# Performance work log

Measured on AMD Instinct MI355X. Metric: run time of the kernel, lower is better.

The kernel has to match this reference:

```python
import jax, jax.numpy as jnp
import numpy as np

MAX_DEG = 6


def neighbor_lookup(atoms, edges, maskvalue, include_self):
    # atoms: (B, A, F), edges: (B, A, D) with -1 padding
    B, A, F = atoms.shape
    D = edges.shape[-1]
    mask = edges >= 0
    idx = jnp.where(mask, edges, 0).reshape(B, A * D)
    g = jnp.take_along_axis(atoms, idx[:, :, None], axis=1).reshape(B, A, D, F)
    g = jnp.where(mask[..., None], g, maskvalue)
    if include_self:
        g = jnp.concatenate([atoms[:, :, None, :], g], axis=2)  # (B,A,D+1,F)
    return g


def graph_conv(atoms, bonds, edges, W, b):
    # W: (MAX_DEG, F_in+BF, C), b: (MAX_DEG, C)
    deg = (edges >= 0).sum(-1)  # (B, A)
    summed_atoms = neighbor_lookup(atoms, edges, 0.0, True).sum(2)  # self + neighbors
    summed_bonds = bonds.sum(2)
    feats = jnp.concatenate([summed_atoms, summed_bonds], axis=-1)
    out = jnp.zeros(feats.shape[:2] + (W.shape[-1],), feats.dtype)
    for d in range(MAX_DEG):  # small fixed loop over degrees
        h = jax.nn.relu(feats @ W[d] + b[d])
        out = out + jnp.where((deg == d)[..., None], h, 0.0)
    return out


def graph_pool(atoms, edges):
    g = neighbor_lookup(atoms, edges, -jnp.inf, True)  # self included -> finite max
    return g.max(axis=2)


def graph_output(atoms, bonds, edges, Wo, bo):
    deg = (edges >= 0).sum(-1)
    feats = jnp.concatenate([atoms, bonds.sum(2)], axis=-1)
    out = jax.nn.softmax(feats @ Wo + bo, axis=-1)
    mask = (deg != 0)[..., None]  # zero out padded atoms
    return jnp.where(mask, out, 0.0).sum(axis=1)  # (B, hid)


def setup_inputs():
    key = jax.random.key(0)
    ks = jax.random.split(key, 16)
    B, A, D = 4096, 64, 6
    AF, BF, H = 37, 6, 128
    s = lambda k, sh: (jax.random.normal(k, sh, jnp.float32) * 0.05)
    return {
        "atoms": jax.random.normal(ks[0], (B, A, AF), jnp.float32),
        "bonds": jax.random.normal(ks[1], (B, A, D, BF), jnp.float32),
        "edges": jax.random.randint(ks[2], (B, A, D), -1, A),
        "W1": s(ks[3], (MAX_DEG, AF + BF, H)),
        "b1": s(ks[4], (MAX_DEG, H)),
        "W2": s(ks[5], (MAX_DEG, H + BF, H)),
        "b2": s(ks[6], (MAX_DEG, H)),
        "Wo": s(ks[7], (H + BF, H)),
        "bo": s(ks[8], (H,)),
        "Wm1": s(ks[9], (H, H // 2)),
        "bm1": s(ks[10], (H // 2,)),
        "Wm2": s(ks[11], (H // 2, H // 4)),
        "bm2": s(ks[12], (H // 4,)),
        "Wm3": s(ks[13], (H // 4, 1)),
        "bm3": s(ks[14], (1,)),
    }


def reference(atoms, bonds, edges, W1, b1, W2, b2, Wo, bo, Wm1, bm1, Wm2, bm2, Wm3, bm3):
    x = graph_conv(atoms, bonds, edges, W1, b1)
    x = graph_pool(x, edges)
    x = graph_conv(x, bonds, edges, W2, b2)
    x = graph_pool(x, edges)
    fp = graph_output(x, bonds, edges, Wo, bo)
    h = jax.nn.relu(fp @ Wm1 + bm1)
    h = jax.nn.relu(h @ Wm2 + bm2)
    out = (h @ Wm3 + bm3).squeeze()  # (B,)
    return out
```

## Files before the change

kernel.cpp:

```cpp
#include <hip/hip_runtime.h>
#include <math.h>


__device__ __forceinline__ float4 max4(float4 a, float4 b) {
  return make_float4(fmaxf(a.x, b.x), fmaxf(a.y, b.y), fmaxf(a.z, b.z), fmaxf(a.w, b.w));
}

__device__ __forceinline__ float4 nbr_max(const float4* sx4, const int* se, int a, int c4) {
  float4 m = sx4[a * 32 + c4];
#pragma unroll
  for (int d = 0; d < 6; ++d) {
    int e = se[a * 6 + d];
    if (e >= 0) m = max4(m, sx4[e * 32 + c4]);
  }
  return m;
}

__device__ __forceinline__ float4 nbr_sum(const float4* sx4, const int* se, int a, int c4) {
  float4 s = sx4[a * 32 + c4];
#pragma unroll
  for (int d = 0; d < 6; ++d) {
    int e = se[a * 6 + d];
    if (e >= 0) {
      float4 v = sx4[e * 32 + c4];
      s.x += v.x; s.y += v.y; s.z += v.z; s.w += v.w;
    }
  }
  return s;
}

__device__ __forceinline__ float4 nbr_wmax(const float4* sx4, const int* se, const int* sdeg,
                                           int a, int c4) {
  float4 m = make_float4(0.f, 0.f, 0.f, 0.f);
  if (sdeg[a] < 6) m = max4(m, sx4[a * 32 + c4]);
#pragma unroll
  for (int d = 0; d < 6; ++d) {
    int e = se[a * 6 + d];
    if (e >= 0 && sdeg[e] < 6) m = max4(m, sx4[e * 32 + c4]);
  }
  return m;
}

__global__ __launch_bounds__(256, 4) void qsar_fused(
    const float* __restrict__ atoms, const float* __restrict__ bonds,
    const int* __restrict__ edges,
    const float* __restrict__ W1, const float* __restrict__ b1,
    const float* __restrict__ W2, const float* __restrict__ b2,
    const float* __restrict__ Wo, const float* __restrict__ bo,
    const float* __restrict__ Wm1, const float* __restrict__ bm1,
    const float* __restrict__ Wm2, const float* __restrict__ bm2,
    const float* __restrict__ Wm3, const float* __restrict__ bm3,
    float* __restrict__ out)
{
  const int b    = blockIdx.x;
  const int tid  = threadIdx.x;
  const int lane = tid & 63;
  const int wid  = tid >> 6;

  __shared__ float s_x[64 * 128];
  __shared__ float s_sa[16 * 38];
  __shared__ float s_bsum[64 * 8];
  __shared__ int   s_edges[64 * 6];
  __shared__ int   s_deg[64];
  __shared__ int   s_work[64];
  __shared__ int   s_perm[64];
  __shared__ float s_rsum[64];
  __shared__ int   s_nwork, s_na, s_nz;

  float4* sx4  = reinterpret_cast<float4*>(s_x);
  float*  s_fp = s_sa;
  float*  s_h1 = s_sa + 256;
  float*  s_h2 = s_sa + 320;

  {
    const int* ge = edges + (size_t)b * (64 * 6);
    for (int i = tid; i < 64 * 6; i += 256) s_edges[i] = ge[i];
    const float* gb = bonds + (size_t)b * (64 * 36);
    for (int i = tid; i < 64 * 6; i += 256) {
      int a = i / 6, f = i - a * 6;
      float s = 0.f;
#pragma unroll
      for (int d = 0; d < 6; ++d) s += gb[a * 36 + d * 6 + f];
      s_bsum[a * 8 + f] = s;
    }
#pragma unroll
    for (int j = 0; j < 8; ++j) sx4[tid + j * 256] = make_float4(0.f, 0.f, 0.f, 0.f);
    if (tid == 0) { s_nwork = 0; s_na = 0; s_nz = 0; }
  }
  __syncthreads();

  if (tid < 64) {
    int dcnt = 0;
#pragma unroll
    for (int d = 0; d < 6; ++d) dcnt += (s_edges[tid * 6 + d] >= 0) ? 1 : 0;
    s_deg[tid] = dcnt;
    if (dcnt < 6) { int p = atomicAdd(&s_nwork, 1); s_work[p] = tid; }
  }
  __syncthreads();

  if (tid < 64) {
    int nzf = (s_deg[tid] < 6) ? 1 : 0;
#pragma unroll
    for (int d = 0; d < 6; ++d) {
      int e = s_edges[tid * 6 + d];
      if (e >= 0 && s_deg[e] < 6) nzf = 1;
    }
    if (nzf) { int p = atomicAdd(&s_na, 1); s_perm[p] = tid; }
    else     { int p = atomicAdd(&s_nz, 1); s_perm[63 - p] = tid; }
  }

  {
    const int nw = s_nwork;
    const float* ga = atoms + (size_t)b * (64 * 37);
    for (int cb = 0; cb < nw; cb += 16) {
      const int cnt = (nw - cb < 16) ? (nw - cb) : 16;
      for (int i = tid; i < cnt * 37; i += 256) {
        int wi = i / 37, k = i - wi * 37;
        int a = s_work[cb + wi];
        float f = ga[a * 37 + k];
#pragma unroll
        for (int d = 0; d < 6; ++d) {
          int e = s_edges[a * 6 + d];
          if (e >= 0) f += ga[e * 37 + k];
        }
        s_sa[wi * 38 + k] = f;
      }
      __syncthreads();
      for (int w = wid; w < cnt; w += 4) {
        const int a = s_work[cb + w];
        const int d = s_deg[a];
        const float* wp = W1 + d * (43 * 128);
        float2 bb = *reinterpret_cast<const float2*>(&b1[d * 128 + 2 * lane]);
        float acc0 = bb.x, acc1 = bb.y;
        for (int k = 0; k < 37; ++k) {
          float f = s_sa[w * 38 + k];
          float2 w2 = *reinterpret_cast<const float2*>(&wp[k * 128 + 2 * lane]);
          acc0 = fmaf(f, w2.x, acc0); acc1 = fmaf(f, w2.y, acc1);
        }
#pragma unroll
        for (int kk = 0; kk < 6; ++kk) {
          float f = s_bsum[a * 8 + kk];
          float2 w2 = *reinterpret_cast<const float2*>(&wp[(37 + kk) * 128 + 2 * lane]);
          acc0 = fmaf(f, w2.x, acc0); acc1 = fmaf(f, w2.y, acc1);
        }
        *reinterpret_cast<float2*>(&s_x[a * 128 + 2 * lane]) =
            make_float2(fmaxf(acc0, 0.f), fmaxf(acc1, 0.f));
      }
      __syncthreads();
    }
  }
  __syncthreads();

  {
    float4 v0 = nbr_max(sx4, s_edges, (tid + 0 * 256) >> 5, tid & 31);
    float4 v1 = nbr_max(sx4, s_edges, (tid + 1 * 256) >> 5, tid & 31);
    float4 v2 = nbr_max(sx4, s_edges, (tid + 2 * 256) >> 5, tid & 31);
    float4 v3 = nbr_max(sx4, s_edges, (tid + 3 * 256) >> 5, tid & 31);
    float4 v4 = nbr_max(sx4, s_edges, (tid + 4 * 256) >> 5, tid & 31);
    float4 v5 = nbr_max(sx4, s_edges, (tid + 5 * 256) >> 5, tid & 31);
    float4 v6 = nbr_max(sx4, s_edges, (tid + 6 * 256) >> 5, tid & 31);
    float4 v7 = nbr_max(sx4, s_edges, (tid + 7 * 256) >> 5, tid & 31);
    __syncthreads();
    sx4[tid + 0 * 256] = v0; sx4[tid + 1 * 256] = v1;
    sx4[tid + 2 * 256] = v2; sx4[tid + 3 * 256] = v3;
    sx4[tid + 4 * 256] = v4; sx4[tid + 5 * 256] = v5;
    sx4[tid + 6 * 256] = v6; sx4[tid + 7 * 256] = v7;
  }
  __syncthreads();

  {
    const float4 z = make_float4(0.f, 0.f, 0.f, 0.f);
    float4 v0 = z, v1 = z, v2 = z, v3 = z, v4 = z, v5 = z, v6 = z, v7 = z;
    if (s_deg[(tid + 0 * 256) >> 5] < 6) v0 = nbr_sum(sx4, s_edges, (tid + 0 * 256) >> 5, tid & 31);
    if (s_deg[(tid + 1 * 256) >> 5] < 6) v1 = nbr_sum(sx4, s_edges, (tid + 1 * 256) >> 5, tid & 31);
    if (s_deg[(tid + 2 * 256) >> 5] < 6) v2 = nbr_sum(sx4, s_edges, (tid + 2 * 256) >> 5, tid & 31);
    if (s_deg[(tid + 3 * 256) >> 5] < 6) v3 = nbr_sum(sx4, s_edges, (tid + 3 * 256) >> 5, tid & 31);
    if (s_deg[(tid + 4 * 256) >> 5] < 6) v4 = nbr_sum(sx4, s_edges, (tid + 4 * 256) >> 5, tid & 31);
    if (s_deg[(tid + 5 * 256) >> 5] < 6) v5 = nbr_sum(sx4, s_edges, (tid + 5 * 256) >> 5, tid & 31);
    if (s_deg[(tid + 6 * 256) >> 5] < 6) v6 = nbr_sum(sx4, s_edges, (tid + 6 * 256) >> 5, tid & 31);
    if (s_deg[(tid + 7 * 256) >> 5] < 6) v7 = nbr_sum(sx4, s_edges, (tid + 7 * 256) >> 5, tid & 31);
    __syncthreads();
    if (s_deg[(tid + 0 * 256) >> 5] < 6) sx4[tid + 0 * 256] = v0;
    if (s_deg[(tid + 1 * 256) >> 5] < 6) sx4[tid + 1 * 256] = v1;
    if (s_deg[(tid + 2 * 256) >> 5] < 6) sx4[tid + 2 * 256] = v2;
    if (s_deg[(tid + 3 * 256) >> 5] < 6) sx4[tid + 3 * 256] = v3;
    if (s_deg[(tid + 4 * 256) >> 5] < 6) sx4[tid + 4 * 256] = v4;
    if (s_deg[(tid + 5 * 256) >> 5] < 6) sx4[tid + 5 * 256] = v5;
    if (s_deg[(tid + 6 * 256) >> 5] < 6) sx4[tid + 6 * 256] = v6;
    if (s_deg[(tid + 7 * 256) >> 5] < 6) sx4[tid + 7 * 256] = v7;
  }
  __syncthreads();

  {
    const int nw = s_nwork;
    for (int w = wid; w < nw; w += 4) {
      const int a = s_work[w];
      const int d = s_deg[a];
      const float* wp = W2 + d * (134 * 128);
      float2 bb = *reinterpret_cast<const float2*>(&b2[d * 128 + 2 * lane]);
      float acc0 = bb.x, acc1 = bb.y;
      for (int k = 0; k < 128; ++k) {
        float f = s_x[a * 128 + k];
        float2 w2 = *reinterpret_cast<const float2*>(&wp[k * 128 + 2 * lane]);
        acc0 = fmaf(f, w2.x, acc0); acc1 = fmaf(f, w2.y, acc1);
      }
#pragma unroll
      for (int kk = 0; kk < 6; ++kk) {
        float f = s_bsum[a * 8 + kk];
        float2 w2 = *reinterpret_cast<const float2*>(&wp[(128 + kk) * 128 + 2 * lane]);
        acc0 = fmaf(f, w2.x, acc0); acc1 = fmaf(f, w2.y, acc1);
      }
      *reinterpret_cast<float2*>(&s_x[a * 128 + 2 * lane]) =
          make_float2(fmaxf(acc0, 0.f), fmaxf(acc1, 0.f));
    }
  }
  __syncthreads();

  {
    float4 v0 = nbr_wmax(sx4, s_edges, s_deg, (tid + 0 * 256) >> 5, tid & 31);
    float4 v1 = nbr_wmax(sx4, s_edges, s_deg, (tid + 1 * 256) >> 5, tid & 31);
    float4 v2 = nbr_wmax(sx4, s_edges, s_deg, (tid + 2 * 256) >> 5, tid & 31);
    float4 v3 = nbr_wmax(sx4, s_edges, s_deg, (tid + 3 * 256) >> 5, tid & 31);
    float4 v4 = nbr_wmax(sx4, s_edges, s_deg, (tid + 4 * 256) >> 5, tid & 31);
    float4 v5 = nbr_wmax(sx4, s_edges, s_deg, (tid + 5 * 256) >> 5, tid & 31);
    float4 v6 = nbr_wmax(sx4, s_edges, s_deg, (tid + 6 * 256) >> 5, tid & 31);
    float4 v7 = nbr_wmax(sx4, s_edges, s_deg, (tid + 7 * 256) >> 5, tid & 31);
    __syncthreads();
    sx4[tid + 0 * 256] = v0; sx4[tid + 1 * 256] = v1;
    sx4[tid + 2 * 256] = v2; sx4[tid + 3 * 256] = v3;
    sx4[tid + 4 * 256] = v4; sx4[tid + 5 * 256] = v5;
    sx4[tid + 6 * 256] = v6; sx4[tid + 7 * 256] = v7;
  }
  __syncthreads();

  {
    const int cg = tid & 31, ag = tid >> 5;
    const int c0 = cg * 4, p0 = ag * 8;
    const int na = s_na;
    int at0 = s_perm[p0 + 0], at1 = s_perm[p0 + 1], at2 = s_perm[p0 + 2], at3 = s_perm[p0 + 3];
    int at4 = s_perm[p0 + 4], at5 = s_perm[p0 + 5], at6 = s_perm[p0 + 6], at7 = s_perm[p0 + 7];
    float acc[8][4];
#pragma unroll
    for (int g = 0; g < 8; ++g) { acc[g][0] = 0.f; acc[g][1] = 0.f; acc[g][2] = 0.f; acc[g][3] = 0.f; }
    if (p0 < na) {
      for (int k = 0; k < 128; ++k) {
        const float4 w4 = *reinterpret_cast<const float4*>(Wo + k * 128 + c0);
        const float f0 = s_x[at0 * 128 + k], f1 = s_x[at1 * 128 + k];
        const float f2 = s_x[at2 * 128 + k], f3 = s_x[at3 * 128 + k];
        const float f4 = s_x[at4 * 128 + k], f5 = s_x[at5 * 128 + k];
        const float f6 = s_x[at6 * 128 + k], f7 = s_x[at7 * 128 + k];
        acc[0][0] = fmaf(f0, w4.x, acc[0][0]); acc[0][1] = fmaf(f0, w4.y, acc[0][1]);
        acc[0][2] = fmaf(f0, w4.z, acc[0][2]); acc[0][3] = fmaf(f0, w4.w, acc[0][3]);
        acc[1][0] = fmaf(f1, w4.x, acc[1][0]); acc[1][1] = fmaf(f1, w4.y, acc[1][1]);
        acc[1][2] = fmaf(f1, w4.z, acc[1][2]); acc[1][3] = fmaf(f1, w4.w, acc[1][3]);
        acc[2][0] = fmaf(f2, w4.x, acc[2][0]); acc[2][1] = fmaf(f2, w4.y, acc[2][1]);
        acc[2][2] = fmaf(f2, w4.z, acc[2][2]); acc[2][3] = fmaf(f2, w4.w, acc[2][3]);
        acc[3][0] = fmaf(f3, w4.x, acc[3][0]); acc[3][1] = fmaf(f3, w4.y, acc[3][1]);
        acc[3][2] = fmaf(f3, w4.z, acc[3][2]); acc[3][3] = fmaf(f3, w4.w, acc[3][3]);
        acc[4][0] = fmaf(f4, w4.x, acc[4][0]); acc[4][1] = fmaf(f4, w4.y, acc[4][1]);
        acc[4][2] = fmaf(f4, w4.z, acc[4][2]); acc[4][3] = fmaf(f4, w4.w, acc[4][3]);
        acc[5][0] = fmaf(f5, w4.x, acc[5][0]); acc[5][1] = fmaf(f5, w4.y, acc[5][1]);
        acc[5][2] = fmaf(f5, w4.z, acc[5][2]); acc[5][3] = fmaf(f5, w4.w, acc[5][3]);
        acc[6][0] = fmaf(f6, w4.x, acc[6][0]); acc[6][1] = fmaf(f6, w4.y, acc[6][1]);
        acc[6][2] = fmaf(f6, w4.z, acc[6][2]); acc[6][3] = fmaf(f6, w4.w, acc[6][3]);
        acc[7][0] = fmaf(f7, w4.x, acc[7][0]); acc[7][1] = fmaf(f7, w4.y, acc[7][1]);
        acc[7][2] = fmaf(f7, w4.z, acc[7][2]); acc[7][3] = fmaf(f7, w4.w, acc[7][3]);
      }
    }
#pragma unroll
    for (int kk = 0; kk < 6; ++kk) {
      const float4 w4 = *reinterpret_cast<const float4*>(Wo + (128 + kk) * 128 + c0);
      const float f0 = s_bsum[at0 * 8 + kk], f1 = s_bsum[at1 * 8 + kk];
      const float f2 = s_bsum[at2 * 8 + kk], f3 = s_bsum[at3 * 8 + kk];
      const float f4 = s_bsum[at4 * 8 + kk], f5 = s_bsum[at5 * 8 + kk];
      const float f6 = s_bsum[at6 * 8 + kk], f7 = s_bsum[at7 * 8 + kk];
      acc[0][0] = fmaf(f0, w4.x, acc[0][0]); acc[0][1] = fmaf(f0, w4.y, acc[0][1]);
      acc[0][2] = fmaf(f0, w4.z, acc[0][2]); acc[0][3] = fmaf(f0, w4.w, acc[0][3]);
      acc[1][0] = fmaf(f1, w4.x, acc[1][0]); acc[1][1] = fmaf(f1, w4.y, acc[1][1]);
      acc[1][2] = fmaf(f1, w4.z, acc[1][2]); acc[1][3] = fmaf(f1, w4.w, acc[1][3]);
      acc[2][0] = fmaf(f2, w4.x, acc[2][0]); acc[2][1] = fmaf(f2, w4.y, acc[2][1]);
      acc[2][2] = fmaf(f2, w4.z, acc[2][2]); acc[2][3] = fmaf(f2, w4.w, acc[2][3]);
      acc[3][0] = fmaf(f3, w4.x, acc[3][0]); acc[3][1] = fmaf(f3, w4.y, acc[3][1]);
      acc[3][2] = fmaf(f3, w4.z, acc[3][2]); acc[3][3] = fmaf(f3, w4.w, acc[3][3]);
      acc[4][0] = fmaf(f4, w4.x, acc[4][0]); acc[4][1] = fmaf(f4, w4.y, acc[4][1]);
      acc[4][2] = fmaf(f4, w4.z, acc[4][2]); acc[4][3] = fmaf(f4, w4.w, acc[4][3]);
      acc[5][0] = fmaf(f5, w4.x, acc[5][0]); acc[5][1] = fmaf(f5, w4.y, acc[5][1]);
      acc[5][2] = fmaf(f5, w4.z, acc[5][2]); acc[5][3] = fmaf(f5, w4.w, acc[5][3]);
      acc[6][0] = fmaf(f6, w4.x, acc[6][0]); acc[6][1] = fmaf(f6, w4.y, acc[6][1]);
      acc[6][2] = fmaf(f6, w4.z, acc[6][2]); acc[6][3] = fmaf(f6, w4.w, acc[6][3]);
      acc[7][0] = fmaf(f7, w4.x, acc[7][0]); acc[7][1] = fmaf(f7, w4.y, acc[7][1]);
      acc[7][2] = fmaf(f7, w4.z, acc[7][2]); acc[7][3] = fmaf(f7, w4.w, acc[7][3]);
    }
    __syncthreads();
    const float4 bo4 = *reinterpret_cast<const float4*>(bo + c0);
    *reinterpret_cast<float4*>(&s_x[at0 * 128 + c0]) =
        make_float4(acc[0][0] + bo4.x, acc[0][1] + bo4.y, acc[0][2] + bo4.z, acc[0][3] + bo4.w);
    *reinterpret_cast<float4*>(&s_x[at1 * 128 + c0]) =
        make_float4(acc[1][0] + bo4.x, acc[1][1] + bo4.y, acc[1][2] + bo4.z, acc[1][3] + bo4.w);
    *reinterpret_cast<float4*>(&s_x[at2 * 128 + c0]) =
        make_float4(acc[2][0] + bo4.x, acc[2][1] + bo4.y, acc[2][2] + bo4.z, acc[2][3] + bo4.w);
    *reinterpret_cast<float4*>(&s_x[at3 * 128 + c0]) =
        make_float4(acc[3][0] + bo4.x, acc[3][1] + bo4.y, acc[3][2] + bo4.z, acc[3][3] + bo4.w);
    *reinterpret_cast<float4*>(&s_x[at4 * 128 + c0]) =
        make_float4(acc[4][0] + bo4.x, acc[4][1] + bo4.y, acc[4][2] + bo4.z, acc[4][3] + bo4.w);
    *reinterpret_cast<float4*>(&s_x[at5 * 128 + c0]) =
        make_float4(acc[5][0] + bo4.x, acc[5][1] + bo4.y, acc[5][2] + bo4.z, acc[5][3] + bo4.w);
    *reinterpret_cast<float4*>(&s_x[at6 * 128 + c0]) =
        make_float4(acc[6][0] + bo4.x, acc[6][1] + bo4.y, acc[6][2] + bo4.z, acc[6][3] + bo4.w);
    *reinterpret_cast<float4*>(&s_x[at7 * 128 + c0]) =
        make_float4(acc[7][0] + bo4.x, acc[7][1] + bo4.y, acc[7][2] + bo4.z, acc[7][3] + bo4.w);
  }
  __syncthreads();

  {
    const int a = tid >> 2, q = tid & 3;
    const int base = a * 128 + q * 32;
    float mx = -3.0e38f;
    for (int j = 0; j < 32; ++j) {
      int jj = (j + tid) & 31;
      mx = fmaxf(mx, s_x[base + jj]);
    }
    mx = fmaxf(mx, __shfl_xor(mx, 1));
    mx = fmaxf(mx, __shfl_xor(mx, 2));
    float sm = 0.f;
    for (int j = 0; j < 32; ++j) {
      int jj = (j + tid) & 31;
      float e = __expf(s_x[base + jj] - mx);
      sm += e;
      s_x[base + jj] = e;
    }
    sm += __shfl_xor(sm, 1);
    sm += __shfl_xor(sm, 2);
    if (q == 0) s_rsum[a] = (s_deg[a] != 0) ? (1.f / sm) : 0.f;
  }
  __syncthreads();

  {
    const int c = tid & 127, half = tid >> 7;
    float s = 0.f;
    for (int a2 = half * 32; a2 < half * 32 + 32; ++a2)
      s = fmaf(s_x[a2 * 128 + c], s_rsum[a2], s);
    s_fp[half * 128 + c] = s;
  }
  __syncthreads();
  if (tid < 128) s_fp[tid] += s_fp[128 + tid];
  __syncthreads();

  if (tid < 64) {
    float acc = bm1[tid];
    for (int k = 0; k < 128; ++k) acc = fmaf(s_fp[k], Wm1[k * 64 + tid], acc);
    s_h1[tid] = fmaxf(acc, 0.f);
  }
  __syncthreads();
  if (tid < 32) {
    float acc = bm2[tid];
    for (int k = 0; k < 64; ++k) acc = fmaf(s_h1[k], Wm2[k * 32 + tid], acc);
    s_h2[tid] = fmaxf(acc, 0.f);
  }
  __syncthreads();
  if (tid < 64) {
    float p = (tid < 32) ? s_h2[tid] * Wm3[tid] : 0.f;
#pragma unroll
    for (int off = 32; off > 0; off >>= 1) p += __shfl_xor(p, off);
    if (tid == 0) out[b] = p + bm3[0];
  }
}

extern "C" void kernel_launch(void* const* d_in, const int* in_sizes, int n_in,
                              void* d_out, int out_size, void* d_ws, size_t ws_size,
                              hipStream_t stream) {
  const float* atoms = (const float*)d_in[0];
  const float* bonds = (const float*)d_in[1];
  const int*   edges = (const int*)d_in[2];
  const float* W1  = (const float*)d_in[3];
  const float* b1  = (const float*)d_in[4];
  const float* W2  = (const float*)d_in[5];
  const float* b2  = (const float*)d_in[6];
  const float* Wo  = (const float*)d_in[7];
  const float* bo  = (const float*)d_in[8];
  const float* Wm1 = (const float*)d_in[9];
  const float* bm1 = (const float*)d_in[10];
  const float* Wm2 = (const float*)d_in[11];
  const float* bm2 = (const float*)d_in[12];
  const float* Wm3 = (const float*)d_in[13];
  const float* bm3 = (const float*)d_in[14];
  float* out = (float*)d_out;

  const int B = out_size;
  qsar_fused<<<dim3(B), dim3(256), 0, stream>>>(
      atoms, bonds, edges, W1, b1, W2, b2, Wo, bo,
      Wm1, bm1, Wm2, bm2, Wm3, bm3, out);
}
```

Measured before the change: 283.6 us.

## Use half-wave float4 tiles in conv GEMVs and restructure output projection

The per-atom conv matvecs now give each atom to a 32-lane half-wave with float4 weight loads, so 8 atoms are in flight instead of 4. The output projection now processes only active atoms in 4-atom tiles, and atoms with all-zero features get a cheap bias-plus-bond-term path. The softmax now uses vectorized float4 LDS reads and writes. These aim to cut LDS and global load instruction count and skip wasted FMA work, at the cost of more weight reloads per atom tile and extra barriers inside the projection loop.

```diff
diff --git a/kernel.cpp b/kernel.cpp
--- a/kernel.cpp
+++ b/kernel.cpp
@@ -54,8 +54,9 @@
 {
   const int b    = blockIdx.x;
   const int tid  = threadIdx.x;
-  const int lane = tid & 63;
   const int wid  = tid >> 6;
+  const int hid  = tid >> 5;
+  const int hl   = tid & 31;
 
   __shared__ float s_x[64 * 128];
   __shared__ float s_sa[16 * 38];
@@ -112,6 +113,7 @@
   {
     const int nw = s_nwork;
     const float* ga = atoms + (size_t)b * (64 * 37);
+    const int c0 = hl * 4;
     for (int cb = 0; cb < nw; cb += 16) {
       const int cnt = (nw - cb < 16) ? (nw - cb) : 16;
       for (int i = tid; i < cnt * 37; i += 256) {
@@ -126,25 +128,28 @@
         s_sa[wi * 38 + k] = f;
       }
       __syncthreads();
-      for (int w = wid; w < cnt; w += 4) {
+      for (int w = hid; w < cnt; w += 8) {
         const int a = s_work[cb + w];
         const int d = s_deg[a];
         const float* wp = W1 + d * (43 * 128);
-        float2 bb = *reinterpret_cast<const float2*>(&b1[d * 128 + 2 * lane]);
-        float acc0 = bb.x, acc1 = bb.y;
+        float4 acc = *reinterpret_cast<const float4*>(&b1[d * 128 + c0]);
+#pragma unroll 4
         for (int k = 0; k < 37; ++k) {
-          float f = s_sa[w * 38 + k];
-          float2 w2 = *reinterpret_cast<const float2*>(&wp[k * 128 + 2 * lane]);
-          acc0 = fmaf(f, w2.x, acc0); acc1 = fmaf(f, w2.y, acc1);
+          const float f = s_sa[w * 38 + k];
+          const float4 w4 = *reinterpret_cast<const float4*>(&wp[k * 128 + c0]);
+          acc.x = fmaf(f, w4.x, acc.x); acc.y = fmaf(f, w4.y, acc.y);
+          acc.z = fmaf(f, w4.z, acc.z); acc.w = fmaf(f, w4.w, acc.w);
         }
 #pragma unroll
         for (int kk = 0; kk < 6; ++kk) {
-          float f = s_bsum[a * 8 + kk];
-          float2 w2 = *reinterpret_cast<const float2*>(&wp[(37 + kk) * 128 + 2 * lane]);
-          acc0 = fmaf(f, w2.x, acc0); acc1 = fmaf(f, w2.y, acc1);
+          const float f = s_bsum[a * 8 + kk];
+          const float4 w4 = *reinterpret_cast<const float4*>(&wp[(37 + kk) * 128 + c0]);
+          acc.x = fmaf(f, w4.x, acc.x); acc.y = fmaf(f, w4.y, acc.y);
+          acc.z = fmaf(f, w4.z, acc.z); acc.w = fmaf(f, w4.w, acc.w);
         }
-        *reinterpret_cast<float2*>(&s_x[a * 128 + 2 * lane]) =
-            make_float2(fmaxf(acc0, 0.f), fmaxf(acc1, 0.f));
+        *reinterpret_cast<float4*>(&s_x[a * 128 + c0]) =
+            make_float4(fmaxf(acc.x, 0.f), fmaxf(acc.y, 0.f),
+                        fmaxf(acc.z, 0.f), fmaxf(acc.w, 0.f));
       }
       __syncthreads();
     }
@@ -193,25 +198,29 @@
 
   {
     const int nw = s_nwork;
-    for (int w = wid; w < nw; w += 4) {
+    const int c0 = hl * 4;
+    for (int w = hid; w < nw; w += 8) {
       const int a = s_work[w];
       const int d = s_deg[a];
       const float* wp = W2 + d * (134 * 128);
-      float2 bb = *reinterpret_cast<const float2*>(&b2[d * 128 + 2 * lane]);
-      float acc0 = bb.x, acc1 = bb.y;
+      float4 acc = *reinterpret_cast<const float4*>(&b2[d * 128 + c0]);
+#pragma unroll 4
       for (int k = 0; k < 128; ++k) {
-        float f = s_x[a * 128 + k];
-        float2 w2 = *reinterpret_cast<const float2*>(&wp[k * 128 + 2 * lane]);
-        acc0 = fmaf(f, w2.x, acc0); acc1 = fmaf(f, w2.y, acc1);
+        const float f = s_x[a * 128 + k];
+        const float4 w4 = *reinterpret_cast<const float4*>(&wp[k * 128 + c0]);
+        acc.x = fmaf(f, w4.x, acc.x); acc.y = fmaf(f, w4.y, acc.y);
+        acc.z = fmaf(f, w4.z, acc.z); acc.w = fmaf(f, w4.w, acc.w);
       }
 #pragma unroll
       for (int kk = 0; kk < 6; ++kk) {
-        float f = s_bsum[a * 8 + kk];
-        float2 w2 = *reinterpret_cast<const float2*>(&wp[(128 + kk) * 128 + 2 * lane]);
-        acc0 = fmaf(f, w2.x, acc0); acc1 = fmaf(f, w2.y, acc1);
+        const float f = s_bsum[a * 8 + kk];
+        const float4 w4 = *reinterpret_cast<const float4*>(&wp[(128 + kk) * 128 + c0]);
+        acc.x = fmaf(f, w4.x, acc.x); acc.y = fmaf(f, w4.y, acc.y);
+        acc.z = fmaf(f, w4.z, acc.z); acc.w = fmaf(f, w4.w, acc.w);
       }
-      *reinterpret_cast<float2*>(&s_x[a * 128 + 2 * lane]) =
-          make_float2(fmaxf(acc0, 0.f), fmaxf(acc1, 0.f));
+      *reinterpret_cast<float4*>(&s_x[a * 128 + c0]) =
+          make_float4(fmaxf(acc.x, 0.f), fmaxf(acc.y, 0.f),
+                      fmaxf(acc.z, 0.f), fmaxf(acc.w, 0.f));
     }
   }
   __syncthreads();
@@ -234,101 +243,119 @@
   __syncthreads();
 
   {
-    const int cg = tid & 31, ag = tid >> 5;
-    const int c0 = cg * 4, p0 = ag * 8;
+    const int cg = tid & 31, ag = hid;
+    const int c0 = cg * 4;
     const int na = s_na;
-    int at0 = s_perm[p0 + 0], at1 = s_perm[p0 + 1], at2 = s_perm[p0 + 2], at3 = s_perm[p0 + 3];
-    int at4 = s_perm[p0 + 4], at5 = s_perm[p0 + 5], at6 = s_perm[p0 + 6], at7 = s_perm[p0 + 7];
-    float acc[8][4];
-#pragma unroll
-    for (int g = 0; g < 8; ++g) { acc[g][0] = 0.f; acc[g][1] = 0.f; acc[g][2] = 0.f; acc[g][3] = 0.f; }
-    if (p0 < na) {
-      for (int k = 0; k < 128; ++k) {
-        const float4 w4 = *reinterpret_cast<const float4*>(Wo + k * 128 + c0);
-        const float f0 = s_x[at0 * 128 + k], f1 = s_x[at1 * 128 + k];
-        const float f2 = s_x[at2 * 128 + k], f3 = s_x[at3 * 128 + k];
-        const float f4 = s_x[at4 * 128 + k], f5 = s_x[at5 * 128 + k];
-        const float f6 = s_x[at6 * 128 + k], f7 = s_x[at7 * 128 + k];
-        acc[0][0] = fmaf(f0, w4.x, acc[0][0]); acc[0][1] = fmaf(f0, w4.y, acc[0][1]);
-        acc[0][2] = fmaf(f0, w4.z, acc[0][2]); acc[0][3] = fmaf(f0, w4.w, acc[0][3]);
-        acc[1][0] = fmaf(f1, w4.x, acc[1][0]); acc[1][1] = fmaf(f1, w4.y, acc[1][1]);
-        acc[1][2] = fmaf(f1, w4.z, acc[1][2]); acc[1][3] = fmaf(f1, w4.w, acc[1][3]);
-        acc[2][0] = fmaf(f2, w4.x, acc[2][0]); acc[2][1] = fmaf(f2, w4.y, acc[2][1]);
-        acc[2][2] = fmaf(f2, w4.z, acc[2][2]); acc[2][3] = fmaf(f2, w4.w, acc[2][3]);
-        acc[3][0] = fmaf(f3, w4.x, acc[3][0]); acc[3][1] = fmaf(f3, w4.y, acc[3][1]);
-        acc[3][2] = fmaf(f3, w4.z, acc[3][2]); acc[3][3] = fmaf(f3, w4.w, acc[3][3]);
-        acc[4][0] = fmaf(f4, w4.x, acc[4][0]); acc[4][1] = fmaf(f4, w4.y, acc[4][1]);
-        acc[4][2] = fmaf(f4, w4.z, acc[4][2]); acc[4][3] = fmaf(f4, w4.w, acc[4][3]);
-        acc[5][0] = fmaf(f5, w4.x, acc[5][0]); acc[5][1] = fmaf(f5, w4.y, acc[5][1]);
-        acc[5][2] = fmaf(f5, w4.z, acc[5][2]); acc[5][3] = fmaf(f5, w4.w, acc[5][3]);
-        acc[6][0] = fmaf(f6, w4.x, acc[6][0]); acc[6][1] = fmaf(f6, w4.y, acc[6][1]);
-        acc[6][2] = fmaf(f6, w4.z, acc[6][2]); acc[6][3] = fmaf(f6, w4.w, acc[6][3]);
-        acc[7][0] = fmaf(f7, w4.x, acc[7][0]); acc[7][1] = fmaf(f7, w4.y, acc[7][1]);
-        acc[7][2] = fmaf(f7, w4.z, acc[7][2]); acc[7][3] = fmaf(f7, w4.w, acc[7][3]);
+    const int nr = (na + 31) >> 5;
+    for (int j = 0; j < nr; ++j) {
+      const int sl = j * 32 + ag * 4;
+      const int at0 = s_perm[sl + 0], at1 = s_perm[sl + 1];
+      const int at2 = s_perm[sl + 2], at3 = s_perm[sl + 3];
+      float a00 = 0.f, a01 = 0.f, a02 = 0.f, a03 = 0.f;
+      float a10 = 0.f, a11 = 0.f, a12 = 0.f, a13 = 0.f;
+      float a20 = 0.f, a21 = 0.f, a22 = 0.f, a23 = 0.f;
+      float a30 = 0.f, a31 = 0.f, a32 = 0.f, a33 = 0.f;
+      if (j * 32 + wid * 8 < na) {
+#pragma unroll 4
+        for (int k = 0; k < 128; ++k) {
+          const float4 w4 = *reinterpret_cast<const float4*>(Wo + k * 128 + c0);
+          const float f0 = s_x[at0 * 128 + k], f1 = s_x[at1 * 128 + k];
+          const float f2 = s_x[at2 * 128 + k], f3 = s_x[at3 * 128 + k];
+          a00 = fmaf(f0, w4.x, a00); a01 = fmaf(f0, w4.y, a01);
+          a02 = fmaf(f0, w4.z, a02); a03 = fmaf(f0, w4.w, a03);
+          a10 = fmaf(f1, w4.x, a10); a11 = fmaf(f1, w4.y, a11);
+          a12 = fmaf(f1, w4.z, a12); a13 = fmaf(f1, w4.w, a13);
+          a20 = fmaf(f2, w4.x, a20); a21 = fmaf(f2, w4.y, a21);
+          a22 = fmaf(f2, w4.z, a22); a23 = fmaf(f2, w4.w, a23);
+          a30 = fmaf(f3, w4.x, a30); a31 = fmaf(f3, w4.y, a31);
+          a32 = fmaf(f3, w4.z, a32); a33 = fmaf(f3, w4.w, a33);
+        }
+#pragma unroll
+        for (int kk = 0; kk < 6; ++kk) {
+          const float4 w4 = *reinterpret_cast<const float4*>(Wo + (128 + kk) * 128 + c0);
+          const float f0 = s_bsum[at0 * 8 + kk], f1 = s_bsum[at1 * 8 + kk];
+          const float f2 = s_bsum[at2 * 8 + kk], f3 = s_bsum[at3 * 8 + kk];
+          a00 = fmaf(f0, w4.x, a00); a01 = fmaf(f0, w4.y, a01);
+          a02 = fmaf(f0, w4.z, a02); a03 = fmaf(f0, w4.w, a03);
+          a10 = fmaf(f1, w4.x, a10); a11 = fmaf(f1, w4.y, a11);
+          a12 = fmaf(f1, w4.z, a12); a13 = fmaf(f1, w4.w, a13);
+          a20 = fmaf(f2, w4.x, a20); a21 = fmaf(f2, w4.y, a21);
+          a22 = fmaf(f2, w4.z, a22); a23 = fmaf(f2, w4.w, a23);
+          a30 = fmaf(f3, w4.x, a30); a31 = fmaf(f3, w4.y, a31);
+          a32 = fmaf(f3, w4.z, a32); a33 = fmaf(f3, w4.w, a33);
+        }
       }
-    }
-#pragma unroll
-    for (int kk = 0; kk < 6; ++kk) {
-      const float4 w4 = *reinterpret_cast<const float4*>(Wo + (128 + kk) * 128 + c0);
-      const float f0 = s_bsum[at0 * 8 + kk], f1 = s_bsum[at1 * 8 + kk];
-      const float f2 = s_bsum[at2 * 8 + kk], f3 = s_bsum[at3 * 8 + kk];
-      const float f4 = s_bsum[at4 * 8 + kk], f5 = s_bsum[at5 * 8 + kk];
-      const float f6 = s_bsum[at6 * 8 + kk], f7 = s_bsum[at7 * 8 + kk];
-      acc[0][0] = fmaf(f0, w4.x, acc[0][0]); acc[0][1] = fmaf(f0, w4.y, acc[0][1]);
-      acc[0][2] = fmaf(f0, w4.z, acc[0][2]); acc[0][3] = fmaf(f0, w4.w, acc[0][3]);
-      acc[1][0] = fmaf(f1, w4.x, acc[1][0]); acc[1][1] = fmaf(f1, w4.y, acc[1][1]);
-      acc[1][2] = fmaf(f1, w4.z, acc[1][2]); acc[1][3] = fmaf(f1, w4.w, acc[1][3]);
-      acc[2][0] = fmaf(f2, w4.x, acc[2][0]); acc[2][1] = fmaf(f2, w4.y, acc[2][1]);
-      acc[2][2] = fmaf(f2, w4.z, acc[2][2]); acc[2][3] = fmaf(f2, w4.w, acc[2][3]);
-      acc[3][0] = fmaf(f3, w4.x, acc[3][0]); acc[3][1] = fmaf(f3, w4.y, acc[3][1]);
-      acc[3][2] = fmaf(f3, w4.z, acc[3][2]); acc[3][3] = fmaf(f3, w4.w, acc[3][3]);
-      acc[4][0] = fmaf(f4, w4.x, acc[4][0]); acc[4][1] = fmaf(f4, w4.y, acc[4][1]);
-      acc[4][2] = fmaf(f4, w4.z, acc[4][2]); acc[4][3] = fmaf(f4, w4.w, acc[4][3]);
-      acc[5][0] = fmaf(f5, w4.x, acc[5][0]); acc[5][1] = fmaf(f5, w4.y, acc[5][1]);
-      acc[5][2] = fmaf(f5, w4.z, acc[5][2]); acc[5][3] = fmaf(f5, w4.w, acc[5][3]);
-      acc[6][0] = fmaf(f6, w4.x, acc[6][0]); acc[6][1] = fmaf(f6, w4.y, acc[6][1]);
-      acc[6][2] = fmaf(f6, w4.z, acc[6][2]); acc[6][3] = fmaf(f6, w4.w, acc[6][3]);
-      acc[7][0] = fmaf(f7, w4.x, acc[7][0]); acc[7][1] = fmaf(f7, w4.y, acc[7][1]);
-      acc[7][2] = fmaf(f7, w4.z, acc[7][2]); acc[7][3] = fmaf(f7, w4.w, acc[7][3]);
-    }
-    __syncthreads();
-    const float4 bo4 = *reinterpret_cast<const float4*>(bo + c0);
-    *reinterpret_cast<float4*>(&s_x[at0 * 128 + c0]) =
-        make_float4(acc[0][0] + bo4.x, acc[0][1] + bo4.y, acc[0][2] + bo4.z, acc[0][3] + bo4.w);
-    *reinterpret_cast<float4*>(&s_x[at1 * 128 + c0]) =
-        make_float4(acc[1][0] + bo4.x, acc[1][1] + bo4.y, acc[1][2] + bo4.z, acc[1][3] + bo4.w);
-    *reinterpret_cast<float4*>(&s_x[at2 * 128 + c0]) =
-        make_float4(acc[2][0] + bo4.x, acc[2][1] + bo4.y, acc[2][2] + bo4.z, acc[2][3] + bo4.w);
-    *reinterpret_cast<float4*>(&s_x[at3 * 128 + c0]) =
-        make_float4(acc[3][0] + bo4.x, acc[3][1] + bo4.y, acc[3][2] + bo4.z, acc[3][3] + bo4.w);
-    *reinterpret_cast<float4*>(&s_x[at4 * 128 + c0]) =
-        make_float4(acc[4][0] + bo4.x, acc[4][1] + bo4.y, acc[4][2] + bo4.z, acc[4][3] + bo4.w);
-    *reinterpret_cast<float4*>(&s_x[at5 * 128 + c0]) =
-        make_float4(acc[5][0] + bo4.x, acc[5][1] + bo4.y, acc[5][2] + bo4.z, acc[5][3] + bo4.w);
-    *reinterpret_cast<float4*>(&s_x[at6 * 128 + c0]) =
-        make_float4(acc[6][0] + bo4.x, acc[6][1] + bo4.y, acc[6][2] + bo4.z, acc[6][3] + bo4.w);
-    *reinterpret_cast<float4*>(&s_x[at7 * 128 + c0]) =
-        make_float4(acc[7][0] + bo4.x, acc[7][1] + bo4.y, acc[7][2] + bo4.z, acc[7][3] + bo4.w);
+      __syncthreads();
+      const float4 bo4 = *reinterpret_cast<const float4*>(bo + c0);
+      if (sl + 0 < na)
+        *reinterpret_cast<float4*>(&s_x[at0 * 128 + c0]) =
+            make_float4(a00 + bo4.x, a01 + bo4.y, a02 + bo4.z, a03 + bo4.w);
+      if (sl + 1 < na)
+        *reinterpret_cast<float4*>(&s_x[at1 * 128 + c0]) =
+            make_float4(a10 + bo4.x, a11 + bo4.y, a12 + bo4.z, a13 + bo4.w);
+      if (sl + 2 < na)
+        *reinterpret_cast<float4*>(&s_x[at2 * 128 + c0]) =
+            make_float4(a20 + bo4.x, a21 + bo4.y, a22 + bo4.z, a23 + bo4.w);
+      if (sl + 3 < na)
+        *reinterpret_cast<float4*>(&s_x[at3 * 128 + c0]) =
+            make_float4(a30 + bo4.x, a31 + bo4.y, a32 + bo4.z, a33 + bo4.w);
+    }
+    const int nz = 64 - na;
+    for (int e = tid; e < nz * 128; e += 256) {
+      int zi = e >> 7, c = e & 127;
+      int a = s_perm[na + zi];
+      float acc = bo[c];
+#pragma unroll
+      for (int kk = 0; kk < 6; ++kk)
+        acc = fmaf(s_bsum[a * 8 + kk], Wo[(128 + kk) * 128 + c], acc);
+      s_x[a * 128 + c] = acc;
+    }
   }
   __syncthreads();
 
   {
     const int a = tid >> 2, q = tid & 3;
-    const int base = a * 128 + q * 32;
-    float mx = -3.0e38f;
-    for (int j = 0; j < 32; ++j) {
-      int jj = (j + tid) & 31;
-      mx = fmaxf(mx, s_x[base + jj]);
-    }
+    float* base = &s_x[a * 128 + q * 32];
+    const float4 v0 = *reinterpret_cast<const float4*>(base + ((0 + tid) & 7) * 4);
+    const float4 v1 = *reinterpret_cast<const float4*>(base + ((1 + tid) & 7) * 4);
+    const float4 v2 = *reinterpret_cast<const float4*>(base + ((2 + tid) & 7) * 4);
+    const float4 v3 = *reinterpret_cast<const float4*>(base + ((3 + tid) & 7) * 4);
+    const float4 v4 = *reinterpret_cast<const float4*>(base + ((4 + tid) & 7) * 4);
+    const float4 v5 = *reinterpret_cast<const float4*>(base + ((5 + tid) & 7) * 4);
+    const float4 v6 = *reinterpret_cast<const float4*>(base + ((6 + tid) & 7) * 4);
+    const float4 v7 = *reinterpret_cast<const float4*>(base + ((7 + tid) & 7) * 4);
+    float mx = fmaxf(fmaxf(fmaxf(v0.x, v0.y), fmaxf(v0.z, v0.w)),
+                     fmaxf(fmaxf(v1.x, v1.y), fmaxf(v1.z, v1.w)));
+    mx = fmaxf(mx, fmaxf(fmaxf(fmaxf(v2.x, v2.y), fmaxf(v2.z, v2.w)),
+                         fmaxf(fmaxf(v3.x, v3.y), fmaxf(v3.z, v3.w))));
+    mx = fmaxf(mx, fmaxf(fmaxf(fmaxf(v4.x, v4.y), fmaxf(v4.z, v4.w)),
+                         fmaxf(fmaxf(v5.x, v5.y), fmaxf(v5.z, v5.w))));
+    mx = fmaxf(mx, fmaxf(fmaxf(fmaxf(v6.x, v6.y), fmaxf(v6.z, v6.w)),
+                         fmaxf(fmaxf(v7.x, v7.y), fmaxf(v7.z, v7.w))));
     mx = fmaxf(mx, __shfl_xor(mx, 1));
     mx = fmaxf(mx, __shfl_xor(mx, 2));
     float sm = 0.f;
-    for (int j = 0; j < 32; ++j) {
-      int jj = (j + tid) & 31;
-      float e = __expf(s_x[base + jj] - mx);
-      sm += e;
-      s_x[base + jj] = e;
-    }
+    float4 e0, e1, e2, e3, e4, e5, e6, e7;
+    e0.x = __expf(v0.x - mx); e0.y = __expf(v0.y - mx); e0.z = __expf(v0.z - mx); e0.w = __expf(v0.w - mx);
+    e1.x = __expf(v1.x - mx); e1.y = __expf(v1.y - mx); e1.z = __expf(v1.z - mx); e1.w = __expf(v1.w - mx);
+    e2.x = __expf(v2.x - mx); e2.y = __expf(v2.y - mx); e2.z = __expf(v2.z - mx); e2.w = __expf(v2.w - mx);
+    e3.x = __expf(v3.x - mx); e3.y = __expf(v3.y - mx); e3.z = __expf(v3.z - mx); e3.w = __expf(v3.w - mx);
+    e4.x = __expf(v4.x - mx); e4.y = __expf(v4.y - mx); e4.z = __expf(v4.z - mx); e4.w = __expf(v4.w - mx);
+    e5.x = __expf(v5.x - mx); e5.y = __expf(v5.y - mx); e5.z = __expf(v5.z - mx); e5.w = __expf(v5.w - mx);
+    e6.x = __expf(v6.x - mx); e6.y = __expf(v6.y - mx); e6.z = __expf(v6.z - mx); e6.w = __expf(v6.w - mx);
+    e7.x = __expf(v7.x - mx); e7.y = __expf(v7.y - mx); e7.z = __expf(v7.z - mx); e7.w = __expf(v7.w - mx);
+    sm += e0.x + e0.y + e0.z + e0.w; sm += e1.x + e1.y + e1.z + e1.w;
+    sm += e2.x + e2.y + e2.z + e2.w; sm += e3.x + e3.y + e3.z + e3.w;
+    sm += e4.x + e4.y + e4.z + e4.w; sm += e5.x + e5.y + e5.z + e5.w;
+    sm += e6.x + e6.y + e6.z + e6.w; sm += e7.x + e7.y + e7.z + e7.w;
+    *reinterpret_cast<float4*>(base + ((0 + tid) & 7) * 4) = e0;
+    *reinterpret_cast<float4*>(base + ((1 + tid) & 7) * 4) = e1;
+    *reinterpret_cast<float4*>(base + ((2 + tid) & 7) * 4) = e2;
+    *reinterpret_cast<float4*>(base + ((3 + tid) & 7) * 4) = e3;
+    *reinterpret_cast<float4*>(base + ((4 + tid) & 7) * 4) = e4;
+    *reinterpret_cast<float4*>(base + ((5 + tid) & 7) * 4) = e5;
+    *reinterpret_cast<float4*>(base + ((6 + tid) & 7) * 4) = e6;
+    *reinterpret_cast<float4*>(base + ((7 + tid) & 7) * 4) = e7;
     sm += __shfl_xor(sm, 1);
     sm += __shfl_xor(sm, 2);
     if (q == 0) s_rsum[a] = (s_deg[a] != 0) ? (1.f / sm) : 0.f;
```

Measured after the change: 245.8 us. 13.3% less time.
